# Performance work log

Hardware: AMD Instinct MI355X
Metric: run time of the kernel (lower is better)

Reference implementation:

```python
import jax, jax.numpy as jnp
import numpy as np

C = 64
G = 4
K = 3
GC = C // G
OS = 1.0  # offset_scale
OM_DIM = int(np.ceil(G * K * K * 3 / 8) * 8)  # 112, padded; only first G*27 used


def setup_inputs() -> dict:
    key = jax.random.key(0)
    ks = jax.random.split(key, 8)
    B, H, W = 2, 384, 384
    s = 0.02
    return {
        "inp": jax.random.normal(ks[0], (B, C, H, W), jnp.float32),
        "Wv": jax.random.normal(ks[1], (C, C), jnp.float32) * s,
        "bv": jnp.zeros((C,), jnp.float32),
        "Wdw": jax.random.normal(ks[2], (C, 1, K, K), jnp.float32) * s,
        "bdw": jnp.zeros((C,), jnp.float32),
        "Wom": jax.random.normal(ks[3], (C, OM_DIM), jnp.float32) * s,
        "bom": jnp.zeros((OM_DIM,), jnp.float32),
        "Wo": jax.random.normal(ks[4], (C, C), jnp.float32) * s,
    }


def _bilinear(v, px, py, H, W, b_idx, g_idx):
    # v: (B,H,W,G,GC); px,py: (B,H,W,G) pixel coords; zero padding outside.
    x0 = jnp.floor(px)
    y0 = jnp.floor(py)
    wx1 = px - x0
    wy1 = py - y0
    x0i = x0.astype(jnp.int32)
    y0i = y0.astype(jnp.int32)
    out = jnp.zeros(px.shape + (v.shape[-1],), v.dtype)
    for dy, wy in ((0, 1.0 - wy1), (1, wy1)):
        for dx, wx in ((0, 1.0 - wx1), (1, wx1)):
            xi = x0i + dx
            yi = y0i + dy
            valid = ((xi >= 0) & (xi < W) & (yi >= 0) & (yi < H)).astype(v.dtype)
            xc = jnp.clip(xi, 0, W - 1)
            yc = jnp.clip(yi, 0, H - 1)
            g = v[b_idx, yc, xc, g_idx]  # (B,H,W,G,GC)
            out = out + g * (wy * wx * valid)[..., None]
    return out


def reference(inp, Wv, bv, Wdw, bdw, Wom, bom, Wo):
    B, _, H, W = inp.shape
    x = inp.transpose(0, 2, 3, 1)  # (B,H,W,C)
    # value projection, split into groups
    value = (x @ Wv + bv).reshape(B, H, W, G, GC)
    # depthwise conv on input feeds the offset/mask predictor
    dw = jax.lax.conv_general_dilated(
        inp, Wdw, window_strides=(1, 1), padding=[(1, 1), (1, 1)],
        feature_group_count=C) + bdw[None, :, None, None]
    om = dw.transpose(0, 2, 3, 1) @ Wom + bom  # (B,H,W,OM_DIM)
    om = om[..., : G * K * K * 3].reshape(B, H, W, G, K * K * 3)
    off = om[..., : K * K * 2].reshape(B, H, W, G, K * K, 2)  # (dx,dy) per point
    mask = om[..., K * K * 2:]  # (B,H,W,G,K*K), no softmax in DCNv4

    base_x = jnp.arange(W, dtype=value.dtype)[None, None, :, None]
    base_y = jnp.arange(H, dtype=value.dtype)[None, :, None, None]
    b_idx = jnp.arange(B)[:, None, None, None]
    g_idx = jnp.arange(G)[None, None, None, :]

    out = jnp.zeros((B, H, W, G, GC), value.dtype)
    k = 0
    for ky in range(K):
        for kx in range(K):
            dx = off[..., k, 0]
            dy = off[..., k, 1]
            px = base_x + ((kx - K // 2) + dx) * OS
            py = base_y + ((ky - K // 2) + dy) * OS
            samp = _bilinear(value, px, py, H, W, b_idx, g_idx)
            out = out + samp * mask[..., k][..., None]
            k += 1

    out = out.reshape(B, H, W, C) @ Wo  # output_proj, no bias (output_bias=False)
    return out.transpose(0, 3, 1, 2)  # back to (B,C,H,W)
```

## Files before the change

### kernel.cpp

```cpp
#include <hip/hip_runtime.h>
#include <hip/hip_bf16.h>
#include <math.h>

namespace {
constexpr int kH = 384, kW = 384, kBn = 2;
constexpr int kHW = kH * kW;
constexpr int kOMD = 112;
constexpr int kNB = kBn * (kHW / 64);
constexpr int kNB8 = kNB / 8;
}

__device__ __forceinline__ int swz(int bid) {
    return (bid & 7) * kNB8 + (bid >> 3);
}

__device__ __forceinline__ void fma4(float* acc, float a, float4 w) {
    acc[0] = fmaf(a, w.x, acc[0]);
    acc[1] = fmaf(a, w.y, acc[1]);
    acc[2] = fmaf(a, w.z, acc[2]);
    acc[3] = fmaf(a, w.w, acc[3]);
}

__device__ __forceinline__ float bl(unsigned u) {
    return __uint_as_float(u << 16);
}
__device__ __forceinline__ float bh(unsigned u) {
    return __uint_as_float(u & 0xffff0000u);
}
__device__ __forceinline__ unsigned short f2bf(float f) {
    union { __hip_bfloat16 b; unsigned short s; } u;
    u.b = __float2bfloat16(f);
    return u.s;
}

__global__ __launch_bounds__(256) void k_value(
        const float* __restrict__ inp, const float* __restrict__ Wv,
        const float* __restrict__ bv, unsigned short* __restrict__ value) {
    __shared__ float xin[64][65];
    __shared__ float wv[64 * 64];
    const int tid = threadIdx.x;
    const int bid = swz(blockIdx.x);
    const int b = bid / (kHW / 64);
    const int pix0 = (bid % (kHW / 64)) * 64;
    const float* ib = inp + (size_t)b * 64 * kHW + pix0;
    for (int i = tid; i < 4096; i += 256) {
        const int c = i >> 6, p = i & 63;
        xin[p][c] = ib[(size_t)c * kHW + p];
        wv[i] = Wv[i];
    }
    __syncthreads();
    const int tc = tid & 15, tp = tid >> 4;
    float acc[4][4];
    {
        const float4 b4 = *(const float4*)(bv + tc * 4);
        #pragma unroll
        for (int q = 0; q < 4; ++q) {
            acc[q][0] = b4.x; acc[q][1] = b4.y; acc[q][2] = b4.z; acc[q][3] = b4.w;
        }
    }
    #pragma unroll 4
    for (int ci = 0; ci < 64; ++ci) {
        const float4 w4 = *(const float4*)&wv[ci * 64 + tc * 4];
        #pragma unroll
        for (int q = 0; q < 4; ++q) {
            fma4(acc[q], xin[tp * 4 + q][ci], w4);
        }
    }
    const int g = tc >> 2, cq = tc & 3;
    #pragma unroll
    for (int q = 0; q < 4; ++q) {
        ushort4 st;
        st.x = f2bf(acc[q][0]); st.y = f2bf(acc[q][1]);
        st.z = f2bf(acc[q][2]); st.w = f2bf(acc[q][3]);
        ushort4* vo = (ushort4*)(value +
                ((size_t)(b * 4 + g) * kHW + pix0 + tp * 4 + q) * 16 + cq * 4);
        *vo = st;
    }
}

__global__ __launch_bounds__(256) void k_main(
        const float* __restrict__ inp, const float* __restrict__ Wdw,
        const float* __restrict__ bdw, const float* __restrict__ Wom,
        const float* __restrict__ bom, const float* __restrict__ Wo,
        const unsigned short* __restrict__ value, float* __restrict__ out) {
    __shared__ float lds1[64][68];

    const int tid = threadIdx.x;
    const int bid = swz(blockIdx.x);
    const int b = bid / (kH * (kW / 64));
    const int rem = bid % (kH * (kW / 64));
    const int h = rem / (kW / 64);
    const int w0 = (rem % (kW / 64)) * 64;

    const int p = tid & 63;
    const int g = tid >> 6;
    const int gs = __builtin_amdgcn_readfirstlane(g);

    {
        const int w = w0 + p;
        #pragma unroll 4
        for (int cc = 0; cc < 16; ++cc) {
            const int c = gs * 16 + cc;
            const float* ib = inp + (size_t)(b * 64 + c) * kHW;
            float s = bdw[c];
            #pragma unroll
            for (int r = 0; r < 3; ++r) {
                const int y = h - 1 + r;
                if (y >= 0 && y < kH) {
                    const float* rowp = ib + (size_t)y * kW;
                    #pragma unroll
                    for (int kx = 0; kx < 3; ++kx) {
                        const int x = w - 1 + kx;
                        const float v = (x >= 0 && x < kW) ? rowp[x] : 0.f;
                        s = fmaf(v, Wdw[c * 9 + r * 3 + kx], s);
                    }
                }
            }
            lds1[c][p] = s;
        }
    }
    __syncthreads();

    float om[27];
    {
        const float* bg = bom + gs * 27;
        #pragma unroll
        for (int j = 0; j < 27; ++j) om[j] = bg[j];
        #pragma unroll 4
        for (int ci = 0; ci < 64; ++ci) {
            const float a = lds1[ci][p];
            const float* wr = Wom + ci * kOMD + gs * 27;
            #pragma unroll
            for (int j = 0; j < 27; ++j) om[j] = fmaf(a, wr[j], om[j]);
        }
    }
    __syncthreads();

    {
        float acc[16];
        #pragma unroll
        for (int j = 0; j < 16; ++j) acc[j] = 0.f;
        const float fw = (float)(w0 + p);
        const float fh = (float)h;
        const unsigned short* vbase = value + (size_t)(b * 4 + gs) * kHW * 16;
        #pragma unroll
        for (int k = 0; k < 9; ++k) {
            const int ky = k / 3, kx = k % 3;
            const float dx = om[2 * k];
            const float dy = om[2 * k + 1];
            const float m = om[18 + k];
            const float px = fw + (float)(kx - 1) + dx;
            const float py = fh + (float)(ky - 1) + dy;
            const float x0f = floorf(px), y0f = floorf(py);
            const int x0 = (int)x0f, y0 = (int)y0f;
            const float wx1 = px - x0f, wy1 = py - y0f;
            const float wx0 = 1.f - wx1, wy0 = 1.f - wy1;
            #pragma unroll
            for (int cor = 0; cor < 4; ++cor) {
                const int dy2 = cor >> 1, dx2 = cor & 1;
                const int xi = x0 + dx2, yi = y0 + dy2;
                float wgt = (dy2 ? wy1 : wy0) * (dx2 ? wx1 : wx0) * m;
                if (xi < 0 || xi >= kW || yi < 0 || yi >= kH) wgt = 0.f;
                const int xc = min(max(xi, 0), kW - 1);
                const int yc = min(max(yi, 0), kH - 1);
                const uint4* vp = (const uint4*)(vbase +
                        ((size_t)yc * kW + xc) * 16);
                const uint4 u0 = vp[0];
                const uint4 u1 = vp[1];
                acc[0]  = fmaf(wgt, bl(u0.x), acc[0]);
                acc[1]  = fmaf(wgt, bh(u0.x), acc[1]);
                acc[2]  = fmaf(wgt, bl(u0.y), acc[2]);
                acc[3]  = fmaf(wgt, bh(u0.y), acc[3]);
                acc[4]  = fmaf(wgt, bl(u0.z), acc[4]);
                acc[5]  = fmaf(wgt, bh(u0.z), acc[5]);
                acc[6]  = fmaf(wgt, bl(u0.w), acc[6]);
                acc[7]  = fmaf(wgt, bh(u0.w), acc[7]);
                acc[8]  = fmaf(wgt, bl(u1.x), acc[8]);
                acc[9]  = fmaf(wgt, bh(u1.x), acc[9]);
                acc[10] = fmaf(wgt, bl(u1.y), acc[10]);
                acc[11] = fmaf(wgt, bh(u1.y), acc[11]);
                acc[12] = fmaf(wgt, bl(u1.z), acc[12]);
                acc[13] = fmaf(wgt, bh(u1.z), acc[13]);
                acc[14] = fmaf(wgt, bl(u1.w), acc[14]);
                acc[15] = fmaf(wgt, bh(u1.w), acc[15]);
            }
        }
        #pragma unroll
        for (int j = 0; j < 16; ++j) lds1[gs * 16 + j][p] = acc[j];
    }
    __syncthreads();

    {
        const int cg = gs;
        float acc[16];
        #pragma unroll
        for (int j = 0; j < 16; ++j) acc[j] = 0.f;
        #pragma unroll 4
        for (int ci = 0; ci < 64; ++ci) {
            const float a = lds1[ci][p];
            const float* wr = Wo + ci * 64 + cg * 16;
            #pragma unroll
            for (int j = 0; j < 16; ++j) acc[j] = fmaf(a, wr[j], acc[j]);
        }
        float* ob = out + (size_t)(b * 64 + cg * 16) * kHW + (size_t)h * kW + w0 + p;
        #pragma unroll
        for (int j = 0; j < 16; ++j) ob[(size_t)j * kHW] = acc[j];
    }
}

extern "C" void kernel_launch(void* const* d_in, const int* in_sizes, int n_in,
                              void* d_out, int out_size, void* d_ws, size_t ws_size,
                              hipStream_t stream) {
    const float* inp = (const float*)d_in[0];
    const float* Wv  = (const float*)d_in[1];
    const float* bv  = (const float*)d_in[2];
    const float* Wdw = (const float*)d_in[3];
    const float* bdw = (const float*)d_in[4];
    const float* Wom = (const float*)d_in[5];
    const float* bom = (const float*)d_in[6];
    const float* Wo  = (const float*)d_in[7];
    float* outp = (float*)d_out;
    unsigned short* value = (unsigned short*)d_ws;

    k_value<<<kNB, 256, 0, stream>>>(inp, Wv, bv, value);
    k_main<<<kNB, 256, 0, stream>>>(inp, Wdw, bdw, Wom, bom, Wo, value, outp);
}
```

Before: 326.9 us.

## Move the value, offset/mask and output projections onto bf16 MFMA

```diff
diff --git a/kernel.cpp b/kernel.cpp
--- a/kernel.cpp
+++ b/kernel.cpp
@@ -8,82 +8,143 @@
 constexpr int kOMD = 112;
 constexpr int kNB = kBn * (kHW / 64);
 constexpr int kNB8 = kNB / 8;
-}
+constexpr size_t kOffWvh = 37748736;
+constexpr size_t kOffWvl = kOffWvh + 8192;
+constexpr size_t kOffWom = kOffWvl + 8192;
+constexpr size_t kOffWot = kOffWom + 14336;
+}
+
+typedef __attribute__((ext_vector_type(8))) short short8;
+typedef __attribute__((ext_vector_type(4))) float f32x4;
 
 __device__ __forceinline__ int swz(int bid) {
     return (bid & 7) * kNB8 + (bid >> 3);
 }
 
-__device__ __forceinline__ void fma4(float* acc, float a, float4 w) {
-    acc[0] = fmaf(a, w.x, acc[0]);
-    acc[1] = fmaf(a, w.y, acc[1]);
-    acc[2] = fmaf(a, w.z, acc[2]);
-    acc[3] = fmaf(a, w.w, acc[3]);
-}
-
-__device__ __forceinline__ float bl(unsigned u) {
-    return __uint_as_float(u << 16);
-}
-__device__ __forceinline__ float bh(unsigned u) {
-    return __uint_as_float(u & 0xffff0000u);
-}
+__device__ __forceinline__ float bl(unsigned u) { return __uint_as_float(u << 16); }
+__device__ __forceinline__ float bh(unsigned u) { return __uint_as_float(u & 0xffff0000u); }
 __device__ __forceinline__ unsigned short f2bf(float f) {
     union { __hip_bfloat16 b; unsigned short s; } u;
     u.b = __float2bfloat16(f);
     return u.s;
 }
+__device__ __forceinline__ float bf2f(unsigned short s) {
+    return __uint_as_float((unsigned)s << 16);
+}
+
+__global__ __launch_bounds__(256) void k_prep(
+        const float* __restrict__ Wv, const float* __restrict__ Wom,
+        const float* __restrict__ Wo, unsigned short* __restrict__ wsu) {
+    unsigned short* Wvh = wsu + kOffWvh / 2;
+    unsigned short* Wvl = wsu + kOffWvl / 2;
+    unsigned short* Wmt = wsu + kOffWom / 2;
+    unsigned short* Wot = wsu + kOffWot / 2;
+    const int tid = blockIdx.x * 256 + threadIdx.x;
+    if (tid < 4096) {
+        const int co = tid >> 6, ci = tid & 63;
+        const float v = Wv[ci * 64 + co];
+        const unsigned short h = f2bf(v);
+        Wvh[co * 64 + ci] = h;
+        Wvl[co * 64 + ci] = f2bf(v - bf2f(h));
+    } else if (tid < 4096 + 7168) {
+        const int i = tid - 4096;
+        const int om = i >> 6, ci = i & 63;
+        Wmt[om * 64 + ci] = f2bf(Wom[ci * kOMD + om]);
+    } else if (tid < 4096 + 7168 + 4096) {
+        const int i = tid - 4096 - 7168;
+        const int co = i >> 6, ci = i & 63;
+        Wot[co * 64 + ci] = f2bf(Wo[ci * 64 + co]);
+    }
+}
 
 __global__ __launch_bounds__(256) void k_value(
-        const float* __restrict__ inp, const float* __restrict__ Wv,
-        const float* __restrict__ bv, unsigned short* __restrict__ value) {
-    __shared__ float xin[64][65];
-    __shared__ float wv[64 * 64];
+        const float* __restrict__ inp, const float* __restrict__ bv,
+        const unsigned short* __restrict__ Wvh, const unsigned short* __restrict__ Wvl,
+        unsigned short* __restrict__ value) {
+    __shared__ __align__(16) char smem[18432];
+    unsigned short* xh = (unsigned short*)smem;
+    unsigned short* xl = xh + 64 * 72;
+    float* vb = (float*)smem;
+
     const int tid = threadIdx.x;
     const int bid = swz(blockIdx.x);
     const int b = bid / (kHW / 64);
     const int pix0 = (bid % (kHW / 64)) * 64;
     const float* ib = inp + (size_t)b * 64 * kHW + pix0;
-    for (int i = tid; i < 4096; i += 256) {
-        const int c = i >> 6, p = i & 63;
-        xin[p][c] = ib[(size_t)c * kHW + p];
-        wv[i] = Wv[i];
-    }
-    __syncthreads();
-    const int tc = tid & 15, tp = tid >> 4;
-    float acc[4][4];
-    {
-        const float4 b4 = *(const float4*)(bv + tc * 4);
-        #pragma unroll
-        for (int q = 0; q < 4; ++q) {
-            acc[q][0] = b4.x; acc[q][1] = b4.y; acc[q][2] = b4.z; acc[q][3] = b4.w;
-        }
-    }
-    #pragma unroll 4
-    for (int ci = 0; ci < 64; ++ci) {
-        const float4 w4 = *(const float4*)&wv[ci * 64 + tc * 4];
-        #pragma unroll
-        for (int q = 0; q < 4; ++q) {
-            fma4(acc[q], xin[tp * 4 + q][ci], w4);
-        }
-    }
-    const int g = tc >> 2, cq = tc & 3;
+
     #pragma unroll
-    for (int q = 0; q < 4; ++q) {
-        ushort4 st;
-        st.x = f2bf(acc[q][0]); st.y = f2bf(acc[q][1]);
-        st.z = f2bf(acc[q][2]); st.w = f2bf(acc[q][3]);
-        ushort4* vo = (ushort4*)(value +
-                ((size_t)(b * 4 + g) * kHW + pix0 + tp * 4 + q) * 16 + cq * 4);
-        *vo = st;
+    for (int j = 0; j < 8; ++j) {
+        const int i = tid + j * 256;
+        const int c2 = i >> 6, p = i & 63;
+        const int c = c2 * 2;
+        const float v0 = ib[(size_t)c * kHW + p];
+        const float v1 = ib[(size_t)(c + 1) * kHW + p];
+        const unsigned short h0 = f2bf(v0), h1 = f2bf(v1);
+        const unsigned short l0 = f2bf(v0 - bf2f(h0));
+        const unsigned short l1 = f2bf(v1 - bf2f(h1));
+        *(unsigned*)&xh[p * 72 + c] = (unsigned)h0 | ((unsigned)h1 << 16);
+        *(unsigned*)&xl[p * 72 + c] = (unsigned)l0 | ((unsigned)l1 << 16);
+    }
+    __syncthreads();
+
+    const int lane = tid & 63, wid = tid >> 6;
+    const int m = lane & 15, quad = lane >> 4;
+    const int row = wid * 16 + m;
+    const short8 ah0 = *(const short8*)&xh[row * 72 + quad * 8];
+    const short8 ah1 = *(const short8*)&xh[row * 72 + 32 + quad * 8];
+    const short8 al0 = *(const short8*)&xl[row * 72 + quad * 8];
+    const short8 al1 = *(const short8*)&xl[row * 72 + 32 + quad * 8];
+    f32x4 accs[4];
+    #pragma unroll
+    for (int nt = 0; nt < 4; ++nt) {
+        const int ncol = nt * 16 + m;
+        const short8 b0 = *(const short8*)&Wvh[ncol * 64 + quad * 8];
+        const short8 b1 = *(const short8*)&Wvh[ncol * 64 + 32 + quad * 8];
+        const short8 c0 = *(const short8*)&Wvl[ncol * 64 + quad * 8];
+        const short8 c1 = *(const short8*)&Wvl[ncol * 64 + 32 + quad * 8];
+        f32x4 acc = {0.f, 0.f, 0.f, 0.f};
+        acc = __builtin_amdgcn_mfma_f32_16x16x32_bf16(ah0, b0, acc, 0, 0, 0);
+        acc = __builtin_amdgcn_mfma_f32_16x16x32_bf16(ah1, b1, acc, 0, 0, 0);
+        acc = __builtin_amdgcn_mfma_f32_16x16x32_bf16(al0, b0, acc, 0, 0, 0);
+        acc = __builtin_amdgcn_mfma_f32_16x16x32_bf16(al1, b1, acc, 0, 0, 0);
+        acc = __builtin_amdgcn_mfma_f32_16x16x32_bf16(ah0, c0, acc, 0, 0, 0);
+        acc = __builtin_amdgcn_mfma_f32_16x16x32_bf16(ah1, c1, acc, 0, 0, 0);
+        accs[nt] = acc;
+    }
+    __syncthreads();
+    #pragma unroll
+    for (int nt = 0; nt < 4; ++nt) {
+        const int co = nt * 16 + m;
+        const float bvn = bv[co];
+        #pragma unroll
+        for (int r = 0; r < 4; ++r) {
+            const int px = wid * 16 + quad * 4 + r;
+            vb[px * 69 + co] = accs[nt][r] + bvn;
+        }
+    }
+    __syncthreads();
+    {
+        const int p = tid & 63, g = tid >> 6;
+        unsigned pk[8];
+        #pragma unroll
+        for (int j = 0; j < 8; ++j) {
+            const float e0 = vb[p * 69 + g * 16 + 2 * j];
+            const float e1 = vb[p * 69 + g * 16 + 2 * j + 1];
+            pk[j] = (unsigned)f2bf(e0) | ((unsigned)f2bf(e1) << 16);
+        }
+        unsigned short* vo = value + ((size_t)(b * 4 + g) * kHW + pix0 + p) * 16;
+        *(uint4*)vo = make_uint4(pk[0], pk[1], pk[2], pk[3]);
+        *((uint4*)vo + 1) = make_uint4(pk[4], pk[5], pk[6], pk[7]);
     }
 }
 
 __global__ __launch_bounds__(256) void k_main(
         const float* __restrict__ inp, const float* __restrict__ Wdw,
-        const float* __restrict__ bdw, const float* __restrict__ Wom,
-        const float* __restrict__ bom, const float* __restrict__ Wo,
+        const float* __restrict__ bdw, const float* __restrict__ bom,
+        const unsigned short* __restrict__ Womt, const unsigned short* __restrict__ Wot,
         const unsigned short* __restrict__ value, float* __restrict__ out) {
-    __shared__ float lds1[64][68];
+    __shared__ __align__(16) unsigned short dwb[64 * 72];
+    __shared__ float omL[64 * 113];
 
     const int tid = threadIdx.x;
     const int bid = swz(blockIdx.x);
@@ -93,21 +154,22 @@
     const int w0 = (rem % (kW / 64)) * 64;
 
     const int p = tid & 63;
-    const int g = tid >> 6;
-    const int gs = __builtin_amdgcn_readfirstlane(g);
+    const int gs = __builtin_amdgcn_readfirstlane(tid >> 6);
+    const int m = p & 15, quad = p >> 4;
 
     {
         const int w = w0 + p;
+        float dwv[16];
         #pragma unroll 4
         for (int cc = 0; cc < 16; ++cc) {
             const int c = gs * 16 + cc;
-            const float* ib = inp + (size_t)(b * 64 + c) * kHW;
+            const float* ibc = inp + (size_t)(b * 64 + c) * kHW;
             float s = bdw[c];
             #pragma unroll
             for (int r = 0; r < 3; ++r) {
                 const int y = h - 1 + r;
                 if (y >= 0 && y < kH) {
-                    const float* rowp = ib + (size_t)y * kW;
+                    const float* rowp = ibc + (size_t)y * kW;
                     #pragma unroll
                     for (int kx = 0; kx < 3; ++kx) {
                         const int x = w - 1 + kx;
@@ -116,27 +178,42 @@
                     }
                 }
             }
-            lds1[c][p] = s;
-        }
-    }
-    __syncthreads();
-
-    float om[27];
-    {
-        const float* bg = bom + gs * 27;
-        #pragma unroll
-        for (int j = 0; j < 27; ++j) om[j] = bg[j];
-        #pragma unroll 4
-        for (int ci = 0; ci < 64; ++ci) {
-            const float a = lds1[ci][p];
-            const float* wr = Wom + ci * kOMD + gs * 27;
+            dwv[cc] = s;
+        }
+        unsigned pk[8];
+        #pragma unroll
+        for (int j = 0; j < 8; ++j)
+            pk[j] = (unsigned)f2bf(dwv[2 * j]) | ((unsigned)f2bf(dwv[2 * j + 1]) << 16);
+        unsigned short* dst = &dwb[p * 72 + gs * 16];
+        *(uint4*)dst = make_uint4(pk[0], pk[1], pk[2], pk[3]);
+        *((uint4*)dst + 1) = make_uint4(pk[4], pk[5], pk[6], pk[7]);
+    }
+    __syncthreads();
+
+    {
+        const int row = gs * 16 + m;
+        const short8 a0 = *(const short8*)&dwb[row * 72 + quad * 8];
+        const short8 a1 = *(const short8*)&dwb[row * 72 + 32 + quad * 8];
+        #pragma unroll
+        for (int nt = 0; nt < 7; ++nt) {
+            const int ncol = nt * 16 + m;
+            const short8 b0 = *(const short8*)&Womt[ncol * 64 + quad * 8];
+            const short8 b1 = *(const short8*)&Womt[ncol * 64 + 32 + quad * 8];
+            const float bias = bom[ncol];
+            f32x4 acc = {bias, bias, bias, bias};
+            acc = __builtin_amdgcn_mfma_f32_16x16x32_bf16(a0, b0, acc, 0, 0, 0);
+            acc = __builtin_amdgcn_mfma_f32_16x16x32_bf16(a1, b1, acc, 0, 0, 0);
             #pragma unroll
-            for (int j = 0; j < 27; ++j) om[j] = fmaf(a, wr[j], om[j]);
-        }
-    }
-    __syncthreads();
-
-    {
+            for (int r = 0; r < 4; ++r)
+                omL[(gs * 16 + quad * 4 + r) * 113 + ncol] = acc[r];
+        }
+    }
+    __syncthreads();
+
+    {
+        float om[27];
+        #pragma unroll
+        for (int j = 0; j < 27; ++j) om[j] = omL[p * 113 + gs * 27 + j];
         float acc[16];
         #pragma unroll
         for (int j = 0; j < 16; ++j) acc[j] = 0.f;
@@ -148,7 +225,7 @@
             const int ky = k / 3, kx = k % 3;
             const float dx = om[2 * k];
             const float dy = om[2 * k + 1];
-            const float m = om[18 + k];
+            const float mk = om[18 + k];
             const float px = fw + (float)(kx - 1) + dx;
             const float py = fh + (float)(ky - 1) + dy;
             const float x0f = floorf(px), y0f = floorf(py);
@@ -159,12 +236,11 @@
             for (int cor = 0; cor < 4; ++cor) {
                 const int dy2 = cor >> 1, dx2 = cor & 1;
                 const int xi = x0 + dx2, yi = y0 + dy2;
-                float wgt = (dy2 ? wy1 : wy0) * (dx2 ? wx1 : wx0) * m;
+                float wgt = (dy2 ? wy1 : wy0) * (dx2 ? wx1 : wx0) * mk;
                 if (xi < 0 || xi >= kW || yi < 0 || yi >= kH) wgt = 0.f;
                 const int xc = min(max(xi, 0), kW - 1);
                 const int yc = min(max(yi, 0), kH - 1);
-                const uint4* vp = (const uint4*)(vbase +
-                        ((size_t)yc * kW + xc) * 16);
+                const uint4* vp = (const uint4*)(vbase + ((size_t)yc * kW + xc) * 16);
                 const uint4 u0 = vp[0];
                 const uint4 u1 = vp[1];
                 acc[0]  = fmaf(wgt, bl(u0.x), acc[0]);
@@ -185,26 +261,32 @@
                 acc[15] = fmaf(wgt, bh(u1.w), acc[15]);
             }
         }
-        #pragma unroll
-        for (int j = 0; j < 16; ++j) lds1[gs * 16 + j][p] = acc[j];
-    }
-    __syncthreads();
-
-    {
-        const int cg = gs;
-        float acc[16];
-        #pragma unroll
-        for (int j = 0; j < 16; ++j) acc[j] = 0.f;
-        #pragma unroll 4
-        for (int ci = 0; ci < 64; ++ci) {
-            const float a = lds1[ci][p];
-            const float* wr = Wo + ci * 64 + cg * 16;
-            #pragma unroll
-            for (int j = 0; j < 16; ++j) acc[j] = fmaf(a, wr[j], acc[j]);
-        }
-        float* ob = out + (size_t)(b * 64 + cg * 16) * kHW + (size_t)h * kW + w0 + p;
-        #pragma unroll
-        for (int j = 0; j < 16; ++j) ob[(size_t)j * kHW] = acc[j];
+        unsigned pk[8];
+        #pragma unroll
+        for (int j = 0; j < 8; ++j)
+            pk[j] = (unsigned)f2bf(acc[2 * j]) | ((unsigned)f2bf(acc[2 * j + 1]) << 16);
+        unsigned short* dst = &dwb[p * 72 + gs * 16];
+        *(uint4*)dst = make_uint4(pk[0], pk[1], pk[2], pk[3]);
+        *((uint4*)dst + 1) = make_uint4(pk[4], pk[5], pk[6], pk[7]);
+    }
+    __syncthreads();
+
+    {
+        const int row = gs * 16 + m;
+        const short8 a0 = *(const short8*)&dwb[row * 72 + quad * 8];
+        const short8 a1 = *(const short8*)&dwb[row * 72 + 32 + quad * 8];
+        #pragma unroll
+        for (int nt = 0; nt < 4; ++nt) {
+            const int ncol = nt * 16 + m;
+            const short8 b0 = *(const short8*)&Wot[ncol * 64 + quad * 8];
+            const short8 b1 = *(const short8*)&Wot[ncol * 64 + 32 + quad * 8];
+            f32x4 acc = {0.f, 0.f, 0.f, 0.f};
+            acc = __builtin_amdgcn_mfma_f32_16x16x32_bf16(a0, b0, acc, 0, 0, 0);
+            acc = __builtin_amdgcn_mfma_f32_16x16x32_bf16(a1, b1, acc, 0, 0, 0);
+            float4 st = make_float4(acc[0], acc[1], acc[2], acc[3]);
+            *(float4*)&out[(size_t)(b * 64 + ncol) * kHW + (size_t)h * kW +
+                           w0 + gs * 16 + quad * 4] = st;
+        }
     }
 }
 
@@ -220,8 +302,14 @@
     const float* bom = (const float*)d_in[6];
     const float* Wo  = (const float*)d_in[7];
     float* outp = (float*)d_out;
-    unsigned short* value = (unsigned short*)d_ws;
-
-    k_value<<<kNB, 256, 0, stream>>>(inp, Wv, bv, value);
-    k_main<<<kNB, 256, 0, stream>>>(inp, Wdw, bdw, Wom, bom, Wo, value, outp);
-}
+    unsigned short* wsu = (unsigned short*)d_ws;
+    unsigned short* value = wsu;
+    const unsigned short* Wvh = wsu + kOffWvh / 2;
+    const unsigned short* Wvl = wsu + kOffWvl / 2;
+    const unsigned short* Wmt = wsu + kOffWom / 2;
+    const unsigned short* Wot = wsu + kOffWot / 2;
+
+    k_prep<<<60, 256, 0, stream>>>(Wv, Wom, Wo, wsu);
+    k_value<<<kNB, 256, 0, stream>>>(inp, bv, Wvh, Wvl, value);
+    k_main<<<kNB, 256, 0, stream>>>(inp, Wdw, bdw, bom, Wmt, Wot, value, outp);
+}
```

After: 432.2 us. 1.32x slower.
